# Kernel tuning notes

Hardware: AMD Instinct MI355X
Metric: run time of the kernel (lower is better)

Reference implementation:

```python
import jax, jax.numpy as jnp
import numpy as np

H = 16          # head_num
DH = 64         # h_size = all_head_size // head_num
HIDDEN = 1024
ALL_HEAD = 1024
B, S = 4, 2048
NEG = -1000000000.0


def setup_inputs() -> dict:
    key = jax.random.key(0)
    ks = jax.random.split(key, 8)
    x = jax.random.normal(ks[0], (B, S, HIDDEN), dtype=jnp.float32)
    y = jax.random.normal(ks[1], (B, S, HIDDEN), dtype=jnp.float32)
    attention_mask = jax.random.randint(ks[2], (B, 1, S, S), 0, 2, dtype=jnp.int32)
    sc = 1.0 / np.sqrt(HIDDEN)
    Wq = jax.random.normal(ks[3], (HIDDEN, ALL_HEAD), dtype=jnp.float32) * sc
    Wk = jax.random.normal(ks[4], (HIDDEN, ALL_HEAD), dtype=jnp.float32) * sc
    Wv = jax.random.normal(ks[5], (HIDDEN, ALL_HEAD), dtype=jnp.float32) * sc
    Wo = jax.random.normal(ks[6], (ALL_HEAD, HIDDEN), dtype=jnp.float32) * (1.0 / np.sqrt(ALL_HEAD))
    bo = jnp.zeros((HIDDEN,), dtype=jnp.float32)
    return {"x": x, "y": y, "Wq": Wq, "Wk": Wk, "Wv": Wv, "Wo": Wo, "bo": bo,
            "attention_mask": attention_mask}


def reference(x, y, Wq, Wk, Wv, Wo, bo, attention_mask):
    b = x.shape[0]
    # projections, split heads: [B, H, S, Dh]
    q = (x @ Wq).reshape(b, -1, H, DH).transpose(0, 2, 1, 3)
    k = (x @ Wk).reshape(b, -1, H, DH).transpose(0, 2, 1, 3)
    v = (y @ Wv).reshape(b, -1, H, DH).transpose(0, 2, 1, 3)
    mask = attention_mask == 0  # True => masked (matches .eq(0))
    scores = jnp.einsum('bhqd,bhkd->bhqk', q, k)
    scores = jnp.where(mask, NEG, scores)  # masked_fill BEFORE scaling, as in source
    attn = jax.nn.softmax(scores / np.sqrt(DH), axis=-1)
    ctx = jnp.einsum('bhqk,bhkd->bhqd', attn, v)
    ctx = ctx.transpose(0, 2, 1, 3).reshape(b, -1, H * DH)
    return ctx @ Wo + bo  # dropout p=0.0 is identity
```

## Files before the change

### kernel.cpp

```cpp
#include <hip/hip_runtime.h>
#include <hip/hip_bf16.h>
#include <stdint.h>

typedef __attribute__((ext_vector_type(8))) short short8;
typedef __attribute__((ext_vector_type(4))) float f32x4;
typedef __attribute__((ext_vector_type(16))) float f32x16;
typedef __hip_bfloat16 bf16;

typedef __attribute__((address_space(3))) uint32_t lds_u32_t;
typedef __attribute__((address_space(1))) const uint32_t glb_u32_t;

__device__ __forceinline__ void gload_lds16(const void* g, void* l) {
  __builtin_amdgcn_global_load_lds((glb_u32_t*)g, (lds_u32_t*)l, 16, 0, 0);
}

__device__ __forceinline__ uint32_t cvt_pk_bf16(float lo, float hi_) {
  uint32_t r;
  asm volatile("v_cvt_pk_bf16_f32 %0, %1, %2" : "=v"(r) : "v"(lo), "v"(hi_));
  return r;
}

__device__ __forceinline__ void plane32swap(uint32_t &a, uint32_t &b) {
  auto r = __builtin_amdgcn_permlane32_swap((int)a, (int)b, false, false);
  a = (uint32_t)r[0]; b = (uint32_t)r[1];
}


__global__ void conv_bf16(const float* __restrict__ in, bf16* __restrict__ outp, int n4) {
  int i = blockIdx.x * blockDim.x + threadIdx.x;
  if (i >= n4) return;
  const float4 v = ((const float4*)in)[i];
  union { ushort4 u; bf16 h[4]; } o;
  o.h[0] = __float2bfloat16(v.x); o.h[1] = __float2bfloat16(v.y);
  o.h[2] = __float2bfloat16(v.z); o.h[3] = __float2bfloat16(v.w);
  ((ushort4*)outp)[i] = o.u;
}

__global__ void transpose_w(const float* __restrict__ W0, const float* __restrict__ W1,
                            const float* __restrict__ W2, const float* __restrict__ W3,
                            bf16* __restrict__ outp) {
  const float* W = blockIdx.z == 0 ? W0 : blockIdx.z == 1 ? W1 : blockIdx.z == 2 ? W2 : W3;
  bf16* o = outp + (size_t)blockIdx.z * 1048576;
  __shared__ float t[32][33];
  int x = threadIdx.x, y0 = threadIdx.y;
  int c0 = blockIdx.x * 32, r0 = blockIdx.y * 32;
#pragma unroll
  for (int i = 0; i < 4; i++)
    t[y0 + i*8][x] = W[(size_t)(r0 + y0 + i*8)*1024 + c0 + x];
  __syncthreads();
#pragma unroll
  for (int i = 0; i < 4; i++)
    o[(size_t)(c0 + y0 + i*8)*1024 + r0 + x] = __float2bfloat16(t[x][y0 + i*8]);
}

__global__ void maskpack(const int* __restrict__ mask, unsigned long long* __restrict__ mbits) {
  int tid = threadIdx.x;
  int lane = tid & 63, wid = tid >> 6;
  size_t word = (size_t)blockIdx.x * 4 + wid;
  int v = mask[word * 64 + lane];
  unsigned long long bits = __ballot(v == 0);
  if (lane == 0) mbits[word] = bits;
}

template<int MODE>
__global__ void gemm_bt(const bf16* __restrict__ A, const bf16* __restrict__ Bt,
                        void* __restrict__ Out, const float* __restrict__ bias) {
  const int tid = threadIdx.x;
  const int lane = tid & 63, wid = tid >> 6;
  const int g = lane >> 4, c = lane & 15;
  const int m0 = blockIdx.x * 128, n0 = blockIdx.y * 128;
  const int wm = wid >> 1, wn = wid & 1;
  __shared__ bf16 As[128 * 64];
  __shared__ bf16 Bs[128 * 64];
  f32x4 acc[4][4] = {};
  for (int k0 = 0; k0 < 1024; k0 += 64) {
#pragma unroll
    for (int i = 0; i < 4; i++) {
      int chunk = wid * 4 + i;
      int idx = chunk * 64 + lane;
      int row = idx >> 3, u = idx & 7;
      int koff = k0 + ((u ^ (row & 7)) * 8);
      gload_lds16(A  + (size_t)(m0 + row) * 1024 + koff, As + chunk * 512);
      gload_lds16(Bt + (size_t)(n0 + row) * 1024 + koff, Bs + chunk * 512);
    }
    __syncthreads();
#pragma unroll
    for (int kk = 0; kk < 2; kk++) {
      short8 af[4], bf_[4];
#pragma unroll
      for (int f = 0; f < 4; f++) {
        int ra = wm * 64 + f * 16 + c;
        af[f]  = *(const short8*)(As + ra * 64 + (((kk * 4 + g) ^ (ra & 7)) * 8));
        int rb = wn * 64 + f * 16 + c;
        bf_[f] = *(const short8*)(Bs + rb * 64 + (((kk * 4 + g) ^ (rb & 7)) * 8));
      }
#pragma unroll
      for (int fm = 0; fm < 4; fm++)
#pragma unroll
        for (int fn = 0; fn < 4; fn++)
          acc[fm][fn] = __builtin_amdgcn_mfma_f32_16x16x32_bf16(af[fm], bf_[fn], acc[fm][fn], 0, 0, 0);
    }
    __syncthreads();
  }
#pragma unroll
  for (int fm = 0; fm < 4; fm++) {
#pragma unroll
    for (int fn = 0; fn < 4; fn++) {
      int gn = n0 + wn * 64 + fn * 16 + c;
#pragma unroll
      for (int r = 0; r < 4; r++) {
        int gm = m0 + wm * 64 + fm * 16 + g * 4 + r;
        float v = acc[fm][fn][r];
        if constexpr (MODE == 2) {
          ((float*)Out)[(size_t)gm * 1024 + gn] = v + bias[gn];
        } else if constexpr (MODE == 0) {
          int b = gm >> 11, s = gm & 2047, hh = gn >> 6, d = gn & 63;
          ((bf16*)Out)[(((size_t)b * 16 + hh) * 2048 + s) * 64 + d] = __float2bfloat16(v);
        } else {
          int b = gm >> 11, s = gm & 2047, hh = gn >> 6, d = gn & 63;
          ((bf16*)Out)[(((size_t)b * 16 + hh) * 64 + d) * 2048 + s] = __float2bfloat16(v);
        }
      }
    }
  }
}

__global__ __launch_bounds__(256, 4) void attn_kernel(
    const bf16* __restrict__ Qb, const bf16* __restrict__ Kb, const bf16* __restrict__ Vt,
    const unsigned long long* __restrict__ mbits, bf16* __restrict__ ctx) {
  const int tid = threadIdx.x;
  const int lane = tid & 63, wid = tid >> 6;
  const int c5 = lane & 31, hi = lane >> 5;
  const int sid = blockIdx.x;
  const int xcd = sid & 7, idx = sid >> 3;
  const int bh = xcd * 8 + (idx >> 4);
  const int qb0 = (idx & 15) * 128 + wid * 32;
  const int b = bh >> 4, h = bh & 15;
  __shared__ bf16 Ks[2][64 * 64];
  __shared__ bf16 Vs[3][64 * 64];
  const bf16* Qp = Qb + (size_t)bh * 2048 * 64;
  const bf16* Kp = Kb + (size_t)bh * 2048 * 64;
  const bf16* Vp = Vt + (size_t)bh * 64 * 2048;
  const unsigned long long* mrow = mbits + ((size_t)b * 2048 + qb0 + c5) * 32;

  auto stage_k = [&](int kt, int sk) {
#pragma unroll
    for (int i = 0; i < 2; i++) {
      int chunk = wid * 2 + i;
      int idx2 = chunk * 64 + lane;
      int row = idx2 >> 3, u = idx2 & 7;
      gload_lds16(Kp + (size_t)(kt * 64 + row) * 64 + ((u ^ (row & 7)) * 8), &Ks[sk][chunk * 512]);
    }
  };
  auto stage_v = [&](int kt, int sv) {
#pragma unroll
    for (int i = 0; i < 2; i++) {
      int chunk = wid * 2 + i;
      int idx2 = chunk * 64 + lane;
      int row = idx2 >> 3, u = idx2 & 7;
      gload_lds16(Vp + (size_t)row * 2048 + kt * 64 + ((u ^ (row & 7)) * 8), &Vs[sv][chunk * 512]);
    }
  };

  short8 qf[4];
#pragma unroll
  for (int ks = 0; ks < 4; ks++)
    qf[ks] = *(const short8*)(Qp + (size_t)(qb0 + c5) * 64 + ks * 16 + hi * 8);

  f32x16 Oacc0 = {}, Oacc1 = {};
  float mrun = -3.0e38f, mc1 = 0.f, lrun = 0.f;
  short8 paP[4];

  const float C1 = 0.18033688011112042f;
  const float THRRAW = 44.36f;

  unsigned long long mwC, mwN;
  stage_k(0, 0);
  stage_v(0, 0);
  mwC = mrow[0];
  __syncthreads();

  int sv = 0, svp = 2;
  for (int kt = 0; kt < 32; kt++) {
    const int sk = kt & 1;
    const int svn = (sv == 2) ? 0 : sv + 1;
    if (kt < 31) { stage_k(kt + 1, sk ^ 1); stage_v(kt + 1, svn); }
    mwN = mrow[(kt + 1) & 31];

    f32x16 s0 = {}, s1 = {};
    __builtin_amdgcn_s_setprio(1);
#pragma unroll
    for (int ks = 0; ks < 4; ks++) {
      short8 aK0 = *(const short8*)(&Ks[sk][(c5)      * 64 + (((ks * 2 + hi) ^ (c5 & 7)) * 8)]);
      short8 aK1 = *(const short8*)(&Ks[sk][(32 + c5) * 64 + (((ks * 2 + hi) ^ (c5 & 7)) * 8)]);
      s0 = __builtin_amdgcn_mfma_f32_32x32x16_bf16(aK0, qf[ks], s0, 0, 0, 0);
      s1 = __builtin_amdgcn_mfma_f32_32x32x16_bf16(aK1, qf[ks], s1, 0, 0, 0);
    }
    if (kt > 0) {
#pragma unroll
      for (int ks = 0; ks < 4; ks++) {
        short8 bV0 = *(const short8*)(&Vs[svp][(c5)      * 64 + (((ks * 2 + hi) ^ (c5 & 7)) * 8)]);
        short8 bV1 = *(const short8*)(&Vs[svp][(32 + c5) * 64 + (((ks * 2 + hi) ^ (c5 & 7)) * 8)]);
        Oacc0 = __builtin_amdgcn_mfma_f32_32x32x16_bf16(paP[ks], bV0, Oacc0, 0, 0, 0);
        Oacc1 = __builtin_amdgcn_mfma_f32_32x32x16_bf16(paP[ks], bV1, Oacc1, 0, 0, 0);
      }
    }
    __builtin_amdgcn_s_setprio(0);
    float lmx = fmaxf(s0[0], s1[0]);
#pragma unroll
    for (int reg = 1; reg < 16; reg++)
      lmx = fmaxf(fmaxf(s0[reg], s1[reg]), lmx);
    if (__any(lmx > mrun + THRRAW)) {
      float rmx = fmaxf(lmx, __shfl_xor(lmx, 32));
      float mnew = fmaxf(mrun, rmx);
      float sc = exp2f((mrun - mnew) * C1);
      mrun = mnew; mc1 = mnew * C1;
      lrun *= sc;
#pragma unroll
      for (int reg = 0; reg < 16; reg++) {
        const int qrow = (reg & 3) + 8 * (reg >> 2) + 4 * hi;
        float srow = __shfl(sc, qrow);
        Oacc0[reg] *= srow; Oacc1[reg] *= srow;
      }
    }
    const uint32_t nlo = ~(((uint32_t)mwC)         >> (4 * hi));
    const uint32_t nhi = ~(((uint32_t)(mwC >> 32)) >> (4 * hi));
    uint32_t pk0[8], pk1[8];
    float lsum = 0.f;
#pragma unroll
    for (int r8 = 0; r8 < 8; r8++) {
      const int rA = 2 * r8, rB = 2 * r8 + 1;
      const int pA = (rA & 3) + 8 * (rA >> 2), pB = (rB & 3) + 8 * (rB >> 2);
      float a0 = exp2f(fmaf(s0[rA], C1, -mc1));
      float a1 = exp2f(fmaf(s0[rB], C1, -mc1));
      float b0 = exp2f(fmaf(s1[rA], C1, -mc1));
      float b1 = exp2f(fmaf(s1[rB], C1, -mc1));
      a0 = __uint_as_float(__float_as_uint(a0) & (uint32_t)(((int32_t)(nlo << (31 - pA))) >> 31));
      a1 = __uint_as_float(__float_as_uint(a1) & (uint32_t)(((int32_t)(nlo << (31 - pB))) >> 31));
      b0 = __uint_as_float(__float_as_uint(b0) & (uint32_t)(((int32_t)(nhi << (31 - pA))) >> 31));
      b1 = __uint_as_float(__float_as_uint(b1) & (uint32_t)(((int32_t)(nhi << (31 - pB))) >> 31));
      lsum += (a0 + a1) + (b0 + b1);
      pk0[r8] = cvt_pk_bf16(a0, a1);
      pk1[r8] = cvt_pk_bf16(b0, b1);
    }
    lrun += lsum;
#pragma unroll
    for (int ks = 0; ks < 4; ks++) {
      const int e0 = 2 * ((2 * ks) & 3);
      const int e1 = 2 * ((2 * ks + 1) & 3);
      uint32_t w0, w1, w2, w3;
      if (ks < 2) { w0 = pk0[e0];     w2 = pk0[e1];
                    w1 = pk0[e0 + 1]; w3 = pk0[e1 + 1]; }
      else        { w0 = pk1[e0];     w2 = pk1[e1];
                    w1 = pk1[e0 + 1]; w3 = pk1[e1 + 1]; }
      plane32swap(w0, w2);
      plane32swap(w1, w3);
      union { uint32_t u[4]; short8 s; } pu;
      pu.u[0] = w0; pu.u[1] = w1; pu.u[2] = w2; pu.u[3] = w3;
      paP[ks] = pu.s;
    }
    mwC = mwN;
    svp = sv; sv = svn;
    __syncthreads();
  }
#pragma unroll
  for (int ks = 0; ks < 4; ks++) {
    short8 bV0 = *(const short8*)(&Vs[svp][(c5)      * 64 + (((ks * 2 + hi) ^ (c5 & 7)) * 8)]);
    short8 bV1 = *(const short8*)(&Vs[svp][(32 + c5) * 64 + (((ks * 2 + hi) ^ (c5 & 7)) * 8)]);
    Oacc0 = __builtin_amdgcn_mfma_f32_32x32x16_bf16(paP[ks], bV0, Oacc0, 0, 0, 0);
    Oacc1 = __builtin_amdgcn_mfma_f32_32x32x16_bf16(paP[ks], bV1, Oacc1, 0, 0, 0);
  }
  float lfull = lrun + __shfl_xor(lrun, 32);
#pragma unroll
  for (int reg = 0; reg < 16; reg++) {
    const int qrow = (reg & 3) + 8 * (reg >> 2) + 4 * hi;
    float linv = __builtin_amdgcn_rcpf(__shfl(lfull, qrow));
    size_t base = ((size_t)b * 2048 + qb0 + qrow) * 1024 + h * 64;
    ctx[base + c5]      = __float2bfloat16(Oacc0[reg] * linv);
    ctx[base + 32 + c5] = __float2bfloat16(Oacc1[reg] * linv);
  }
}


extern "C" void kernel_launch(void* const* d_in, const int* in_sizes, int n_in,
                              void* d_out, int out_size, void* d_ws, size_t ws_size,
                              hipStream_t stream) {
  const float* x  = (const float*)d_in[0];
  const float* y  = (const float*)d_in[1];
  const float* Wq = (const float*)d_in[2];
  const float* Wk = (const float*)d_in[3];
  const float* Wv = (const float*)d_in[4];
  const float* Wo = (const float*)d_in[5];
  const float* bo = (const float*)d_in[6];
  const int* amask = (const int*)d_in[7];
  float* out = (float*)d_out;

  char* ws = (char*)d_ws;
  bf16* xb = (bf16*)ws;
  bf16* yb = (bf16*)(ws + 16777216);
  bf16* WT = (bf16*)(ws + 33554432);
  bf16* Qb = (bf16*)(ws + 41943040);
  bf16* Kb = (bf16*)(ws + 58720256);
  bf16* Vt = (bf16*)(ws + 75497472);
  unsigned long long* mbits = (unsigned long long*)(ws + 92274688);
  bf16* ctx = xb;

  conv_bf16<<<8192, 256, 0, stream>>>(x, xb, 2097152);
  conv_bf16<<<8192, 256, 0, stream>>>(y, yb, 2097152);
  transpose_w<<<dim3(32, 32, 4), dim3(32, 8), 0, stream>>>(Wq, Wk, Wv, Wo, WT);
  maskpack<<<65536, 256, 0, stream>>>(amask, mbits);

  dim3 gg(64, 8);
  gemm_bt<0><<<gg, 256, 0, stream>>>(xb, WT + 0 * 1048576, Qb, nullptr);
  gemm_bt<0><<<gg, 256, 0, stream>>>(xb, WT + 1 * 1048576, Kb, nullptr);
  gemm_bt<1><<<gg, 256, 0, stream>>>(yb, WT + 2 * 1048576, Vt, nullptr);

  attn_kernel<<<1024, 256, 0, stream>>>(Qb, Kb, Vt, mbits, ctx);

  gemm_bt<2><<<gg, 256, 0, stream>>>(ctx, WT + 3 * 1048576, out, bo);
}
```

Measured before the change: 285.9 us.

## Compute softmax row sums via MFMA with ones vector, use raw exp2 and sbfe masking

Replaces the per-lane VALU row-sum accumulation of softmax probabilities with an extra MFMA per k-step that multiplies the bf16 probability tile by a ones vector. The row sum then lands in the same layout as the output accumulator, which removes the final shuffles. It also swaps exp2f for the raw hardware exp2 intrinsic and uses sbfe to build the mask bits. The sums now come from bf16-rounded probabilities, which matches the numerator, but the extra MFMA adds matrix-core work and 16 more accumulator registers.

After: 278.4 us. -2.6%, faster.

```diff
diff --git a/kernel.cpp b/kernel.cpp
--- a/kernel.cpp
+++ b/kernel.cpp
@@ -167,8 +167,12 @@
   for (int ks = 0; ks < 4; ks++)
     qf[ks] = *(const short8*)(Qp + (size_t)(qb0 + c5) * 64 + ks * 16 + hi * 8);
 
-  f32x16 Oacc0 = {}, Oacc1 = {};
-  float mrun = -3.0e38f, mc1 = 0.f, lrun = 0.f;
+  short8 onesf;
+#pragma unroll
+  for (int j = 0; j < 8; j++) onesf[j] = (short)0x3F80;
+
+  f32x16 Oacc0 = {}, Oacc1 = {}, accL = {};
+  float mrun = -3.0e38f, mc1 = 0.f;
   short8 paP[4];
 
   const float C1 = 0.18033688011112042f;
@@ -203,6 +207,7 @@
         short8 bV1 = *(const short8*)(&Vs[svp][(32 + c5) * 64 + (((ks * 2 + hi) ^ (c5 & 7)) * 8)]);
         Oacc0 = __builtin_amdgcn_mfma_f32_32x32x16_bf16(paP[ks], bV0, Oacc0, 0, 0, 0);
         Oacc1 = __builtin_amdgcn_mfma_f32_32x32x16_bf16(paP[ks], bV1, Oacc1, 0, 0, 0);
+        accL  = __builtin_amdgcn_mfma_f32_32x32x16_bf16(paP[ks], onesf, accL, 0, 0, 0);
       }
     }
     __builtin_amdgcn_s_setprio(0);
@@ -213,37 +218,33 @@
     if (__any(lmx > mrun + THRRAW)) {
       float rmx = fmaxf(lmx, __shfl_xor(lmx, 32));
       float mnew = fmaxf(mrun, rmx);
-      float sc = exp2f((mrun - mnew) * C1);
+      float sc = __builtin_amdgcn_exp2f((mrun - mnew) * C1);
       mrun = mnew; mc1 = mnew * C1;
-      lrun *= sc;
 #pragma unroll
       for (int reg = 0; reg < 16; reg++) {
         const int qrow = (reg & 3) + 8 * (reg >> 2) + 4 * hi;
         float srow = __shfl(sc, qrow);
-        Oacc0[reg] *= srow; Oacc1[reg] *= srow;
+        Oacc0[reg] *= srow; Oacc1[reg] *= srow; accL[reg] *= srow;
       }
     }
     const uint32_t nlo = ~(((uint32_t)mwC)         >> (4 * hi));
     const uint32_t nhi = ~(((uint32_t)(mwC >> 32)) >> (4 * hi));
     uint32_t pk0[8], pk1[8];
-    float lsum = 0.f;
 #pragma unroll
     for (int r8 = 0; r8 < 8; r8++) {
       const int rA = 2 * r8, rB = 2 * r8 + 1;
       const int pA = (rA & 3) + 8 * (rA >> 2), pB = (rB & 3) + 8 * (rB >> 2);
-      float a0 = exp2f(fmaf(s0[rA], C1, -mc1));
-      float a1 = exp2f(fmaf(s0[rB], C1, -mc1));
-      float b0 = exp2f(fmaf(s1[rA], C1, -mc1));
-      float b1 = exp2f(fmaf(s1[rB], C1, -mc1));
-      a0 = __uint_as_float(__float_as_uint(a0) & (uint32_t)(((int32_t)(nlo << (31 - pA))) >> 31));
-      a1 = __uint_as_float(__float_as_uint(a1) & (uint32_t)(((int32_t)(nlo << (31 - pB))) >> 31));
-      b0 = __uint_as_float(__float_as_uint(b0) & (uint32_t)(((int32_t)(nhi << (31 - pA))) >> 31));
-      b1 = __uint_as_float(__float_as_uint(b1) & (uint32_t)(((int32_t)(nhi << (31 - pB))) >> 31));
-      lsum += (a0 + a1) + (b0 + b1);
+      float a0 = __builtin_amdgcn_exp2f(fmaf(s0[rA], C1, -mc1));
+      float a1 = __builtin_amdgcn_exp2f(fmaf(s0[rB], C1, -mc1));
+      float b0 = __builtin_amdgcn_exp2f(fmaf(s1[rA], C1, -mc1));
+      float b1 = __builtin_amdgcn_exp2f(fmaf(s1[rB], C1, -mc1));
+      a0 = __uint_as_float(__float_as_uint(a0) & (uint32_t)__builtin_amdgcn_sbfe(nlo, pA, 1));
+      a1 = __uint_as_float(__float_as_uint(a1) & (uint32_t)__builtin_amdgcn_sbfe(nlo, pB, 1));
+      b0 = __uint_as_float(__float_as_uint(b0) & (uint32_t)__builtin_amdgcn_sbfe(nhi, pA, 1));
+      b1 = __uint_as_float(__float_as_uint(b1) & (uint32_t)__builtin_amdgcn_sbfe(nhi, pB, 1));
       pk0[r8] = cvt_pk_bf16(a0, a1);
       pk1[r8] = cvt_pk_bf16(b0, b1);
     }
-    lrun += lsum;
 #pragma unroll
     for (int ks = 0; ks < 4; ks++) {
       const int e0 = 2 * ((2 * ks) & 3);
@@ -269,12 +270,12 @@
     short8 bV1 = *(const short8*)(&Vs[svp][(32 + c5) * 64 + (((ks * 2 + hi) ^ (c5 & 7)) * 8)]);
     Oacc0 = __builtin_amdgcn_mfma_f32_32x32x16_bf16(paP[ks], bV0, Oacc0, 0, 0, 0);
     Oacc1 = __builtin_amdgcn_mfma_f32_32x32x16_bf16(paP[ks], bV1, Oacc1, 0, 0, 0);
-  }
-  float lfull = lrun + __shfl_xor(lrun, 32);
+    accL  = __builtin_amdgcn_mfma_f32_32x32x16_bf16(paP[ks], onesf, accL, 0, 0, 0);
+  }
 #pragma unroll
   for (int reg = 0; reg < 16; reg++) {
     const int qrow = (reg & 3) + 8 * (reg >> 2) + 4 * hi;
-    float linv = __builtin_amdgcn_rcpf(__shfl(lfull, qrow));
+    float linv = __builtin_amdgcn_rcpf(accL[reg]);
     size_t base = ((size_t)b * 2048 + qb0 + qrow) * 1024 + h * 64;
     ctx[base + c5]      = __float2bfloat16(Oacc0[reg] * linv);
     ctx[base + 32 + c5] = __float2bfloat16(Oacc1[reg] * linv);
```
